# Kernel tuning notes

Hardware: AMD Instinct MI355X
Metric: run time of the kernel (lower is better)

Reference implementation:

```python
import jax, jax.numpy as jnp
import numpy as np
import math
from jax import lax

B, C, T = 32, 256, 1024
KS = 64          # key_size
KERN = 3         # conv kernel size
PAD = 2          # (KERN-1)*dilation, chomped -> causal left pad
SQRT_KS = math.sqrt(KS)


def setup_inputs() -> dict:
    key = jax.random.key(0)
    ks = jax.random.split(key, 14)
    s = 0.01
    return {
        "x":  jax.random.normal(ks[0], (B, C, T), jnp.float32),
        # attention linears (stored [in, out])
        "wq": jax.random.normal(ks[1], (C, KS), jnp.float32) * s,
        "bq": jnp.zeros((KS,), jnp.float32),
        "wk": jax.random.normal(ks[2], (C, KS), jnp.float32) * s,
        "bk": jnp.zeros((KS,), jnp.float32),
        "wv": jax.random.normal(ks[3], (C, C), jnp.float32) * s,
        "bv": jnp.zeros((C,), jnp.float32),
        # weight-normed conv 1: v [out,in,k], g [out], b [out]
        "v1": jax.random.normal(ks[4], (C, C, KERN), jnp.float32) * s,
        "g1": jnp.ones((C,), jnp.float32),
        "b1": jnp.zeros((C,), jnp.float32),
        # weight-normed conv 2
        "v2": jax.random.normal(ks[5], (C, C, KERN), jnp.float32) * s,
        "g2": jnp.ones((C,), jnp.float32),
        "b2": jnp.zeros((C,), jnp.float32),
    }


def _wn_conv_relu(h, v, g, b):
    # weight_norm (dim=0): W = g * v / ||v||, norm over (in, k) per out channel
    norm = jnp.sqrt(jnp.sum(v * v, axis=(1, 2), keepdims=True))
    W = (g[:, None, None] / norm) * v
    # left-pad PAD == Conv1d(padding=PAD) + Chomp1d(PAD)  (causal conv)
    y = lax.conv_general_dilated(h, W, window_strides=(1,), padding=[(PAD, 0)],
                                 dimension_numbers=("NCH", "OIH", "NCH"))
    return jax.nn.relu(y + b[None, :, None])


def reference(x, wq, bq, wk, bk, wv, bv, v1, g1, b1, v2, g2, b2):
    t = x.shape[2]
    xt = jnp.swapaxes(x, 1, 2)                      # [B, T, C]
    q = xt @ wq + bq                                # [B, T, KS]
    k = xt @ wk + bk                                # [B, T, KS]
    v = xt @ wv + bv                                # [B, T, C]
    scores = jnp.einsum("bqd,bkd->bqk", q, k)       # [B, Tq, Tk]
    # torch mask[j][i] = 1 if i > j -> masked where key index > query index
    idx = jnp.arange(t)
    mask = idx[None, :] > idx[:, None]              # [Tq, Tk]
    scores = jnp.where(mask[None], -jnp.inf, scores)
    # NOTE: source applies softmax over dim=1 (the QUERY axis) — faithful quirk
    attn = jax.nn.softmax(scores / SQRT_KS, axis=1)  # [B, Tq, Tk]
    out_attn = jnp.einsum("bqk,bkc->bqc", attn, v)  # [B, T, C]
    out_attn = jnp.swapaxes(out_attn, 1, 2)         # [B, C, T]
    # conv stack (dropout=0 / eval)
    out = _wn_conv_relu(out_attn, v1, g1, b1)
    out = _wn_conv_relu(out, v2, g2, b2)
    # en_res branch: per-timestep scaling of x by softmaxed attention mass
    weight_x = jax.nn.softmax(jnp.sum(attn, axis=2), axis=1)  # [B, T]
    en_res_x = weight_x[:, None, :] * x                       # [B, C, T]
    # downsample is None (n_inputs == n_outputs)
    return jax.nn.relu(out + x + en_res_x)
```

## Files before the change

kernel.cpp:

```cpp
#include <hip/hip_runtime.h>
#include <math.h>

#define BB 32
#define CC 256
#define TT 1024

typedef __attribute__((ext_vector_type(4))) float f4;
typedef __attribute__((ext_vector_type(4))) float f32x4;
typedef __attribute__((ext_vector_type(16))) float f32x16;
typedef __attribute__((ext_vector_type(8))) short s8;
typedef __attribute__((ext_vector_type(4))) short s4v;

__device__ inline short f2bf(float f) {
    unsigned u = __builtin_bit_cast(unsigned, f);
    u = (u + 0x7FFFu + ((u >> 16) & 1u)) >> 16;
    return (short)u;
}

static const size_t OFF_QBF  = 0;
static const size_t OFF_KBF  = 4194304;
static const size_t OFF_VT   = 8388608;
static const size_t OFF_OA   = 25165824;
static const size_t OFF_C1   = 58720256;
static const size_t OFF_CRZ  = 75497472;
static const size_t OFF_RS   = 75628544;
static const size_t OFF_WX   = 75759616;
static const size_t OFF_W1   = 75890688;
static const size_t OFF_W2   = 76283904;
static const size_t OFF_WQKV = 76677120;

__global__ __launch_bounds__(256)
void wn_kernel(const float* __restrict__ v1, const float* __restrict__ g1,
               const float* __restrict__ v2, const float* __restrict__ g2,
               short* __restrict__ w1bf, short* __restrict__ w2bf) {
    __shared__ float red[4];
    int which = blockIdx.x >> 8, o = blockIdx.x & 255;
    const float* v = which ? v2 : v1;
    const float* g = which ? g2 : g1;
    short* wt = which ? w2bf : w1bf;
    const float* row = v + (size_t)o * 768;
    int tid = threadIdx.x, lane = tid & 63, wv_ = tid >> 6;
    float r0 = row[tid], r1 = row[tid + 256], r2 = row[tid + 512];
    float s = r0 * r0 + r1 * r1 + r2 * r2;
    for (int d = 1; d < 64; d <<= 1) s += __shfl_xor(s, d, 64);
    if (lane == 0) red[wv_] = s;
    __syncthreads();
    float scale = g[o] * rsqrtf(red[0] + red[1] + red[2] + red[3]);
    for (int j = 0; j < 3; ++j)
        wt[((size_t)(j * 256 + o)) * 256 + tid] = f2bf(scale * row[tid * 3 + j]);
}

__global__ __launch_bounds__(256)
void pack_kernel(const float* __restrict__ wq, const float* __restrict__ wk,
                 const float* __restrict__ wv, short* __restrict__ wqkvbf) {
    int n = blockIdx.x * 4 + (threadIdx.x >> 6);
    int c0 = (threadIdx.x & 63) * 4;
    for (int p = 0; p < 4; ++p) {
        int c = c0 + p;
        float w;
        if (n < 64)       w = wq[c * 64 + n];
        else if (n < 128) w = wk[c * 64 + n - 64];
        else              w = wv[c * 256 + n - 128];
        wqkvbf[(size_t)n * 256 + c] = f2bf(w);
    }
}

__global__ void transpose_kernel(const float* __restrict__ x, short* __restrict__ xt) {
    __shared__ float Tt[64 * 68];
    int tid = threadIdx.x;
    int c0 = blockIdx.x * 64, t0 = blockIdx.y * 64, b = blockIdx.z;
    for (int it = 0; it < 4; ++it) {
        int idx = tid + 256 * it;
        int cr = idx >> 4, tc = idx & 15;
        f4 v = *reinterpret_cast<const f4*>(&x[((size_t)b * CC + c0 + cr) * TT + t0 + tc * 4]);
        *reinterpret_cast<f4*>(&Tt[cr * 68 + tc * 4]) = v;
    }
    __syncthreads();
    for (int it = 0; it < 2; ++it) {
        int idx = tid + 256 * it;
        int tl = idx >> 3, seg = idx & 7;
        s8 o;
        for (int p = 0; p < 8; ++p) o[p] = f2bf(Tt[(seg * 8 + p) * 68 + tl]);
        *reinterpret_cast<s8*>(&xt[((size_t)b * TT + t0 + tl) * CC + c0 + seg * 8]) = o;
    }
}

__global__ __launch_bounds__(256, 3)
void qkv_kernel(const short* __restrict__ xt, const short* __restrict__ wqkv,
                const float* __restrict__ bq, const float* __restrict__ bk,
                const float* __restrict__ bv,
                short* __restrict__ qbf, short* __restrict__ kbf, short* __restrict__ vt) {
    __shared__ short SL[128 * 72 + 64 * 72];
    short* Asm = SL;
    short* Bsm = SL + 128 * 72;
    int tid = threadIdx.x, wv_ = tid >> 6, lane = tid & 63;
    int n15 = lane & 15, quad = lane >> 4;
    int bid = blockIdx.x;
    int r = bid & 7, n = (bid >> 3) % 6, qd = bid / 48;
    int bt = qd * 8 + r;
    int b = bt >> 3, t0 = (bt & 7) * 128;
    int n0 = n * 64;

    f32x4 acc[2][4];
    for (int i = 0; i < 2; ++i) for (int j = 0; j < 4; ++j)
        for (int p = 0; p < 4; ++p) acc[i][j][p] = 0.f;

    for (int kc = 0; kc < 4; ++kc) {
        int c0 = kc * 64;
        __syncthreads();
        for (int it = 0; it < 4; ++it) {
            int idx = tid + 256 * it;
            int row = idx >> 3, seg = idx & 7;
            *reinterpret_cast<s8*>(&Asm[row * 72 + seg * 8]) =
                *reinterpret_cast<const s8*>(&xt[((size_t)b * TT + t0 + row) * CC + c0 + seg * 8]);
        }
        for (int it = 0; it < 2; ++it) {
            int idx = tid + 256 * it;
            int row = idx >> 3, seg = idx & 7;
            *reinterpret_cast<s8*>(&Bsm[row * 72 + seg * 8]) =
                *reinterpret_cast<const s8*>(&wqkv[(size_t)(n0 + row) * 256 + c0 + seg * 8]);
        }
        __syncthreads();
        for (int ks = 0; ks < 2; ++ks)
            for (int mt2 = 0; mt2 < 2; ++mt2) {
                s8 a = *reinterpret_cast<const s8*>(&Asm[(wv_ * 32 + mt2 * 16 + n15) * 72 + quad * 8 + ks * 32]);
                for (int nt = 0; nt < 4; ++nt) {
                    s8 bb = *reinterpret_cast<const s8*>(&Bsm[(nt * 16 + n15) * 72 + quad * 8 + ks * 32]);
                    acc[mt2][nt] = __builtin_amdgcn_mfma_f32_16x16x32_bf16(a, bb, acc[mt2][nt], 0, 0, 0);
                }
            }
    }
    if (n0 < 128) {
        short* outp = (n0 == 0) ? qbf : kbf;
        const float* bias = (n0 == 0) ? bq : bk;
        for (int mt2 = 0; mt2 < 2; ++mt2)
            for (int nt = 0; nt < 4; ++nt) {
                int n_ = nt * 16 + n15;
                float bvl = bias[n_];
                for (int reg = 0; reg < 4; ++reg) {
                    int t = t0 + wv_ * 32 + mt2 * 16 + quad * 4 + reg;
                    outp[((size_t)b * TT + t) * 64 + n_] = f2bf(acc[mt2][nt][reg] + bvl);
                }
            }
    } else {
        int cbase = n0 - 128;
        __syncthreads();
        short* Tw = SL + wv_ * 3072;
        for (int mt2 = 0; mt2 < 2; ++mt2)
            for (int nt = 0; nt < 4; ++nt) {
                int n_ = nt * 16 + n15;
                float bvl = bv[cbase + n_];
                for (int reg = 0; reg < 4; ++reg)
                    Tw[n_ * 48 + mt2 * 16 + quad * 4 + reg] = f2bf(acc[mt2][nt][reg] + bvl);
            }
        for (int p = 0; p < 4; ++p) {
            int n_ = (lane >> 2) + 16 * p;
            int seg = lane & 3;
            s8 vv = *reinterpret_cast<const s8*>(&Tw[n_ * 48 + seg * 8]);
            *reinterpret_cast<s8*>(&vt[((size_t)b * CC + cbase + n_) * TT + t0 + wv_ * 32 + seg * 8]) = vv;
        }
    }
}

__global__ __launch_bounds__(512, 2)
void colz_kernel(const short* __restrict__ qbf, const short* __restrict__ kbf,
                 float* __restrict__ colrz) {
    __shared__ short Qs[64 * 72], Ks[64 * 72];
    __shared__ float redz[8 * 32];
    int tid = threadIdx.x, wv_ = tid >> 6, lane = tid & 63;
    int l31 = lane & 31, lh = lane >> 5;
    int qhalf = wv_ & 1, khalf = (wv_ >> 1) & 1, w4 = wv_ >> 2;
    int bid = blockIdx.x;
    int half = bid >> 8;
    int idx = bid & 255;
    int b = idx >> 3, pr = idx & 7;
    int kt = half ? (15 - pr) : pr;
    int row = tid >> 3, sg = (tid & 7) * 8;

    s8 kr0 = *reinterpret_cast<const s8*>(&kbf[((size_t)b * TT + kt * 64 + row) * 64 + sg]);
    s8 qr0 = *reinterpret_cast<const s8*>(&qbf[((size_t)b * TT + kt * 64 + row) * 64 + sg]);
    float zloc = 0.f;
    for (int qt = kt; qt < 16; ++qt) {
        __syncthreads();
        if (qt == kt) *reinterpret_cast<s8*>(&Ks[row * 72 + sg]) = kr0;
        *reinterpret_cast<s8*>(&Qs[row * 72 + sg]) = qr0;
        __syncthreads();
        if (qt < 15)
            qr0 = *reinterpret_cast<const s8*>(&qbf[((size_t)b * TT + (qt + 1) * 64 + row) * 64 + sg]);
        f32x16 s;
        for (int p = 0; p < 16; ++p) s[p] = 0.f;
        for (int kc = 0; kc < 4; ++kc) {
            s8 a  = *reinterpret_cast<const s8*>(&Qs[(qhalf * 32 + l31) * 72 + kc * 16 + lh * 8]);
            s8 bb = *reinterpret_cast<const s8*>(&Ks[(khalf * 32 + l31) * 72 + kc * 16 + lh * 8]);
            s = __builtin_amdgcn_mfma_f32_32x32x16_bf16(a, bb, s, 0, 0, 0);
        }
        int kg = kt * 64 + khalf * 32 + l31;
        int qb0 = qt * 64 + qhalf * 32 + 4 * lh;
        if (qt > kt) {
            for (int r = 0; r < 8; ++r) {
                int reg = w4 * 8 + r;
                zloc += __expf(s[reg] * 0.125f);
            }
        } else {
            for (int r = 0; r < 8; ++r) {
                int reg = w4 * 8 + r;
                if (qb0 + (reg & 3) + 8 * (reg >> 2) >= kg) zloc += __expf(s[reg] * 0.125f);
            }
        }
    }
    float zc = zloc + __shfl_xor(zloc, 32, 64);
    if (lane < 32) redz[wv_ * 32 + lane] = zc;
    __syncthreads();
    if (tid < 64) {
        int kh = tid >> 5, kk = tid & 31;
        float Z;
        if (kh == 0) Z = redz[0 * 32 + kk] + redz[1 * 32 + kk] + redz[4 * 32 + kk] + redz[5 * 32 + kk];
        else         Z = redz[2 * 32 + kk] + redz[3 * 32 + kk] + redz[6 * 32 + kk] + redz[7 * 32 + kk];
        colrz[(size_t)b * TT + kt * 64 + tid] = 1.0f / Z;
    }
}

__global__ __launch_bounds__(512, 2)
void attn_kernel(const short* __restrict__ qbf, const short* __restrict__ kbf,
                 const short* __restrict__ vt, const float* __restrict__ colrz,
                 short* __restrict__ oab, float* __restrict__ rowsum) {
    __shared__ short Qs[64 * 72];
    __shared__ short Ks[64 * 72];
    __shared__ short Ps[64 * 72];
    __shared__ short Vs[256 * 72];
    __shared__ float redR[2][64];
    int tid = threadIdx.x, wv_ = tid >> 6, lane = tid & 63;
    int l31 = lane & 31, lh = lane >> 5;
    int wq2 = wv_ & 1, wk2 = (wv_ >> 1) & 1, w4 = wv_ >> 2, wcq = wv_ >> 1;
    int bid = blockIdx.x;
    int half = bid >> 8;
    int idx = bid & 255;
    int b = idx >> 3, pr = idx & 7;
    int qt = half ? pr : (15 - pr);
    int row = tid >> 3, sg = (tid & 7) * 8;

    s8 kreg, vreg[4];
    {
        kreg = *reinterpret_cast<const s8*>(&kbf[((size_t)b * TT + row) * 64 + sg]);
        for (int it = 0; it < 4; ++it) {
            int idx2 = tid + 512 * it;
            int vr = idx2 >> 3, seg = idx2 & 7;
            vreg[it] = *reinterpret_cast<const s8*>(&vt[((size_t)b * CC + vr) * TT + seg * 8]);
        }
    }

    s8 qr0 = *reinterpret_cast<const s8*>(&qbf[((size_t)b * TT + qt * 64 + row) * 64 + sg]);
    f32x16 acc[2];
    for (int i = 0; i < 2; ++i) for (int p = 0; p < 16; ++p) acc[i][p] = 0.f;
    float rsum[8];
    for (int i = 0; i < 8; ++i) rsum[i] = 0.f;

    for (int kt = 0; kt <= qt; ++kt) {
        __syncthreads();
        if (kt == 0) *reinterpret_cast<s8*>(&Qs[row * 72 + sg]) = qr0;
        *reinterpret_cast<s8*>(&Ks[row * 72 + sg]) = kreg;
        for (int it = 0; it < 4; ++it) {
            int idx2 = tid + 512 * it;
            int vr = idx2 >> 3, seg = idx2 & 7;
            *reinterpret_cast<s8*>(&Vs[vr * 72 + seg * 8]) = vreg[it];
        }
        __syncthreads();
        int nkt = (kt < qt) ? kt + 1 : -1;
        if (nkt >= 0) {
            kreg = *reinterpret_cast<const s8*>(&kbf[((size_t)b * TT + nkt * 64 + row) * 64 + sg]);
            for (int it = 0; it < 4; ++it) {
                int idx2 = tid + 512 * it;
                int vr = idx2 >> 3, seg = idx2 & 7;
                vreg[it] = *reinterpret_cast<const s8*>(&vt[((size_t)b * CC + vr) * TT + nkt * 64 + seg * 8]);
            }
        }
        f32x16 s;
        for (int p = 0; p < 16; ++p) s[p] = 0.f;
        for (int kc = 0; kc < 4; ++kc) {
            s8 a  = *reinterpret_cast<const s8*>(&Qs[(wq2 * 32 + l31) * 72 + kc * 16 + lh * 8]);
            s8 bb = *reinterpret_cast<const s8*>(&Ks[(wk2 * 32 + l31) * 72 + kc * 16 + lh * 8]);
            s = __builtin_amdgcn_mfma_f32_32x32x16_bf16(a, bb, s, 0, 0, 0);
        }
        int kg = kt * 64 + wk2 * 32 + l31;
        float rz = colrz[(size_t)b * TT + kg];
        bool full = (kt < qt);
        int qb0 = qt * 64 + wq2 * 32 + 4 * lh;
        for (int r = 0; r < 8; ++r) {
            int reg = w4 * 8 + r;
            int rr = (reg & 3) + 8 * (reg >> 2);
            float p = 0.f;
            if (full || qb0 + rr >= kg) p = __expf(s[reg] * 0.125f) * rz;
            rsum[r] += p;
            Ps[(wq2 * 32 + rr + 4 * lh) * 72 + wk2 * 32 + l31] = f2bf(p);
        }
        __syncthreads();
        for (int kc = 0; kc < 4; ++kc) {
            s8 a = *reinterpret_cast<const s8*>(&Ps[(wq2 * 32 + l31) * 72 + kc * 16 + lh * 8]);
            for (int nt = 0; nt < 2; ++nt) {
                s8 bb = *reinterpret_cast<const s8*>(&Vs[(wcq * 64 + nt * 32 + l31) * 72 + kc * 16 + lh * 8]);
                acc[nt] = __builtin_amdgcn_mfma_f32_32x32x16_bf16(a, bb, acc[nt], 0, 0, 0);
            }
        }
    }
    for (int r = 0; r < 8; ++r) {
        float v = rsum[r];
        v += __shfl_xor(v, 1, 64);
        v += __shfl_xor(v, 2, 64);
        v += __shfl_xor(v, 4, 64);
        v += __shfl_xor(v, 8, 64);
        v += __shfl_xor(v, 16, 64);
        int reg = w4 * 8 + r;
        int rr = (reg & 3) + 8 * (reg >> 2);
        if (l31 == 0) redR[wk2][wq2 * 32 + rr + 4 * lh] = v;
    }
    for (int nt = 0; nt < 2; ++nt) {
        int c = wcq * 64 + nt * 32 + l31;
        for (int reg = 0; reg < 16; ++reg) {
            int q = qt * 64 + wq2 * 32 + (reg & 3) + 8 * (reg >> 2) + 4 * lh;
            oab[((size_t)b * TT + q) * CC + c] = f2bf(acc[nt][reg]);
        }
    }
    __syncthreads();
    if (tid < 64) rowsum[(size_t)b * TT + qt * 64 + tid] = redR[0][tid] + redR[1][tid];
}

__global__ __launch_bounds__(256, 3)
void conv_kernel(const void* __restrict__ inp, int in_is_fp32,
                 const short* __restrict__ wbf, const float* __restrict__ bias,
                 void* __restrict__ outp, int out_is_bf16,
                 const float* __restrict__ xres, const float* __restrict__ wxv,
                 int fuse_final) {
    __shared__ short SL[130 * 72 + 3 * 64 * 72];
    short* As = SL;
    short* Bs = SL + 130 * 72;
    int tid = threadIdx.x, wv_ = tid >> 6, lane = tid & 63;
    int n15 = lane & 15, quad = lane >> 4;
    int bid = blockIdx.x;
    int r = bid & 7;
    int n0 = ((bid >> 3) & 3) << 6;
    int bm = (bid >> 5) * 8 + r;
    int b = bm >> 3, mt = bm & 7;
    int t0 = mt * 128;
    f32x4 acc[2][4];
    for (int i = 0; i < 2; ++i) for (int j = 0; j < 4; ++j)
        for (int p = 0; p < 4; ++p) acc[i][j][p] = 0.f;

    for (int kc = 0; kc < 4; ++kc) {
        int c0 = kc * 64;
        __syncthreads();
        if (in_is_fp32) {
            const float* in = (const float*)inp;
            for (int it = 0; it < 9; ++it) {
                int idx = tid + 256 * it;
                int row = idx >> 4, fc = idx & 15;
                if (row < 130) {
                    int t = t0 + row - 2;
                    s4v st;
                    if (t >= 0) {
                        f4 v = *reinterpret_cast<const f4*>(&in[((size_t)b * TT + t) * CC + c0 + fc * 4]);
                        for (int p = 0; p < 4; ++p) st[p] = f2bf(v[p]);
                    } else { for (int p = 0; p < 4; ++p) st[p] = 0; }
                    *reinterpret_cast<s4v*>(&As[row * 72 + fc * 4]) = st;
                }
            }
        } else {
            const short* in = (const short*)inp;
            for (int it = 0; it < 5; ++it) {
                int idx = tid + 256 * it;
                int row = idx >> 3, seg = idx & 7;
                if (row < 130) {
                    int t = t0 + row - 2;
                    s8 st;
                    if (t >= 0) st = *reinterpret_cast<const s8*>(&in[((size_t)b * TT + t) * CC + c0 + seg * 8]);
                    else for (int p = 0; p < 8; ++p) st[p] = 0;
                    *reinterpret_cast<s8*>(&As[row * 72 + seg * 8]) = st;
                }
            }
        }
        for (int it = 0; it < 6; ++it) {
            int idx = tid + 256 * it;
            int row = idx >> 3, seg = idx & 7;
            int j = row >> 6, o = row & 63;
            *reinterpret_cast<s8*>(&Bs[row * 72 + seg * 8]) =
                *reinterpret_cast<const s8*>(&wbf[((size_t)(j * 256 + n0 + o)) * 256 + c0 + seg * 8]);
        }
        __syncthreads();
        for (int j = 0; j < 3; ++j)
            for (int ks = 0; ks < 2; ++ks)
                for (int mt2 = 0; mt2 < 2; ++mt2) {
                    s8 a = *reinterpret_cast<const s8*>(&As[(wv_ * 32 + mt2 * 16 + n15 + j) * 72 + quad * 8 + ks * 32]);
                    for (int nt = 0; nt < 4; ++nt) {
                        s8 bb = *reinterpret_cast<const s8*>(&Bs[(j * 64 + nt * 16 + n15) * 72 + quad * 8 + ks * 32]);
                        acc[mt2][nt] = __builtin_amdgcn_mfma_f32_16x16x32_bf16(a, bb, acc[mt2][nt], 0, 0, 0);
                    }
                }
    }
    if (!fuse_final) {
        for (int mt2 = 0; mt2 < 2; ++mt2)
            for (int nt = 0; nt < 4; ++nt) {
                int o = n0 + nt * 16 + n15;
                float bvl = bias[o];
                for (int reg = 0; reg < 4; ++reg) {
                    int t = t0 + wv_ * 32 + mt2 * 16 + quad * 4 + reg;
                    float v = fmaxf(acc[mt2][nt][reg] + bvl, 0.f);
                    if (out_is_bf16) ((short*)outp)[((size_t)b * TT + t) * CC + o] = f2bf(v);
                    else             ((float*)outp)[((size_t)b * TT + t) * CC + o] = v;
                }
            }
    } else {
        float* Ft = (float*)SL;
        __syncthreads();
        for (int mt2 = 0; mt2 < 2; ++mt2)
            for (int nt = 0; nt < 4; ++nt) {
                int ol = nt * 16 + n15;
                float bvl = bias[n0 + ol];
                for (int reg = 0; reg < 4; ++reg) {
                    int tl = wv_ * 32 + mt2 * 16 + quad * 4 + reg;
                    Ft[tl * 67 + ol] = fmaxf(acc[mt2][nt][reg] + bvl, 0.f);
                }
            }
        __syncthreads();
        int c_l = tid >> 5;
        int t_l = (tid & 31) * 4;
        f4 wv4 = *reinterpret_cast<const f4*>(&wxv[(size_t)b * TT + t0 + t_l]);
        for (int pass = 0; pass < 8; ++pass) {
            int c = n0 + pass * 8 + c_l;
            f4 xv = *reinterpret_cast<const f4*>(&xres[((size_t)b * CC + c) * TT + t0 + t_l]);
            f4 rr;
            for (int p = 0; p < 4; ++p)
                rr[p] = fmaxf(Ft[(t_l + p) * 67 + pass * 8 + c_l] + xv[p] * (1.f + wv4[p]), 0.f);
            *reinterpret_cast<f4*>(&((float*)outp)[((size_t)b * CC + c) * TT + t0 + t_l]) = rr;
        }
    }
}

__global__ void rowsm_kernel(const float* __restrict__ rowsum, float* __restrict__ wx) {
    __shared__ float red[256];
    int b = blockIdx.x, tid = threadIdx.x;
    float v[4];
    float m = -1e30f;
    for (int r = 0; r < 4; ++r) { v[r] = rowsum[(size_t)b * TT + tid + 256 * r]; m = fmaxf(m, v[r]); }
    red[tid] = m; __syncthreads();
    for (int s = 128; s > 0; s >>= 1) { if (tid < s) red[tid] = fmaxf(red[tid], red[tid + s]); __syncthreads(); }
    m = red[0]; __syncthreads();
    float e[4], zs = 0.f;
    for (int r = 0; r < 4; ++r) { e[r] = __expf(v[r] - m); zs += e[r]; }
    red[tid] = zs; __syncthreads();
    for (int s = 128; s > 0; s >>= 1) { if (tid < s) red[tid] += red[tid + s]; __syncthreads(); }
    float rz = 1.0f / red[0];
    for (int r = 0; r < 4; ++r) wx[(size_t)b * TT + tid + 256 * r] = e[r] * rz;
}

extern "C" void kernel_launch(void* const* d_in, const int* in_sizes, int n_in,
                              void* d_out, int out_size, void* d_ws, size_t ws_size,
                              hipStream_t stream) {
    (void)in_sizes; (void)n_in; (void)out_size; (void)ws_size;
    const float* x  = (const float*)d_in[0];
    const float* wq = (const float*)d_in[1];
    const float* bq = (const float*)d_in[2];
    const float* wk = (const float*)d_in[3];
    const float* bk = (const float*)d_in[4];
    const float* wv = (const float*)d_in[5];
    const float* bv = (const float*)d_in[6];
    const float* v1 = (const float*)d_in[7];
    const float* g1 = (const float*)d_in[8];
    const float* b1 = (const float*)d_in[9];
    const float* v2 = (const float*)d_in[10];
    const float* g2 = (const float*)d_in[11];
    const float* b2 = (const float*)d_in[12];
    char* ws = (char*)d_ws;
    float* out = (float*)d_out;

    short* qbf  = (short*)(ws + OFF_QBF);
    short* kbf  = (short*)(ws + OFF_KBF);
    short* vt   = (short*)(ws + OFF_VT);
    short* xt   = (short*)(ws + OFF_OA);
    short* oab  = (short*)(ws + OFF_OA);
    short* c1   = (short*)(ws + OFF_C1);
    float* crz  = (float*)(ws + OFF_CRZ);
    float* rs   = (float*)(ws + OFF_RS);
    float* wxb  = (float*)(ws + OFF_WX);
    short* w1bf = (short*)(ws + OFF_W1);
    short* w2bf = (short*)(ws + OFF_W2);
    short* wqkv = (short*)(ws + OFF_WQKV);

    wn_kernel<<<dim3(512), dim3(256), 0, stream>>>(v1, g1, v2, g2, w1bf, w2bf);
    pack_kernel<<<dim3(96), dim3(256), 0, stream>>>(wq, wk, wv, wqkv);
    transpose_kernel<<<dim3(4, 16, 32), dim3(256), 0, stream>>>(x, xt);
    qkv_kernel<<<dim3(1536), dim3(256), 0, stream>>>(xt, wqkv, bq, bk, bv, qbf, kbf, vt);
    colz_kernel<<<dim3(512), dim3(512), 0, stream>>>(qbf, kbf, crz);
    attn_kernel<<<dim3(512), dim3(512), 0, stream>>>(qbf, kbf, vt, crz, oab, rs);
    rowsm_kernel<<<dim3(32), dim3(256), 0, stream>>>(rs, wxb);
    conv_kernel<<<dim3(1024), dim3(256), 0, stream>>>(oab, 0, w1bf, b1, c1, 1,
                                                      nullptr, nullptr, 0);
    conv_kernel<<<dim3(1024), dim3(256), 0, stream>>>(c1, 0, w2bf, b2, out, 0,
                                                      x, wxb, 1);
}
```

Measured before the change: 251.8 us.

## Restructure attention and column-normalizer kernels to load MFMA fragments from global directly

Both colz and attn kernels now read Q/K/V MFMA operand fragments straight from global memory into registers, dropping the shared-memory staging of Q, K and V. Each block now handles two paired tiles (pr and 15-pr) for causal load balance, and the query tile is split into 32-row halves across blocks. attn uses a double-buffered P tile with one barrier per iteration, and launch bounds go up to four blocks per SM for occupancy. In exchange, K and V fragments are re-read from global/L2 by more blocks and waves, and the exp work is spread across duplicate waves.

```diff
diff --git a/kernel.cpp b/kernel.cpp
--- a/kernel.cpp
+++ b/kernel.cpp
@@ -162,166 +162,151 @@
     }
 }
 
-__global__ __launch_bounds__(512, 2)
+__global__ __launch_bounds__(512, 4)
 void colz_kernel(const short* __restrict__ qbf, const short* __restrict__ kbf,
                  float* __restrict__ colrz) {
-    __shared__ short Qs[64 * 72], Ks[64 * 72];
     __shared__ float redz[8 * 32];
     int tid = threadIdx.x, wv_ = tid >> 6, lane = tid & 63;
     int l31 = lane & 31, lh = lane >> 5;
-    int qhalf = wv_ & 1, khalf = (wv_ >> 1) & 1, w4 = wv_ >> 2;
+    int qhf = wv_ & 1, wdup = wv_ >> 1;
     int bid = blockIdx.x;
-    int half = bid >> 8;
+    int kh = bid >> 8;
     int idx = bid & 255;
     int b = idx >> 3, pr = idx & 7;
-    int kt = half ? (15 - pr) : pr;
-    int row = tid >> 3, sg = (tid & 7) * 8;
-
-    s8 kr0 = *reinterpret_cast<const s8*>(&kbf[((size_t)b * TT + kt * 64 + row) * 64 + sg]);
-    s8 qr0 = *reinterpret_cast<const s8*>(&qbf[((size_t)b * TT + kt * 64 + row) * 64 + sg]);
-    float zloc = 0.f;
-    for (int qt = kt; qt < 16; ++qt) {
-        __syncthreads();
-        if (qt == kt) *reinterpret_cast<s8*>(&Ks[row * 72 + sg]) = kr0;
-        *reinterpret_cast<s8*>(&Qs[row * 72 + sg]) = qr0;
-        __syncthreads();
-        if (qt < 15)
-            qr0 = *reinterpret_cast<const s8*>(&qbf[((size_t)b * TT + (qt + 1) * 64 + row) * 64 + sg]);
-        f32x16 s;
-        for (int p = 0; p < 16; ++p) s[p] = 0.f;
-        for (int kc = 0; kc < 4; ++kc) {
-            s8 a  = *reinterpret_cast<const s8*>(&Qs[(qhalf * 32 + l31) * 72 + kc * 16 + lh * 8]);
-            s8 bb = *reinterpret_cast<const s8*>(&Ks[(khalf * 32 + l31) * 72 + kc * 16 + lh * 8]);
-            s = __builtin_amdgcn_mfma_f32_32x32x16_bf16(a, bb, s, 0, 0, 0);
-        }
-        int kg = kt * 64 + khalf * 32 + l31;
-        int qb0 = qt * 64 + qhalf * 32 + 4 * lh;
-        if (qt > kt) {
-            for (int r = 0; r < 8; ++r) {
-                int reg = w4 * 8 + r;
-                zloc += __expf(s[reg] * 0.125f);
-            }
-        } else {
-            for (int r = 0; r < 8; ++r) {
-                int reg = w4 * 8 + r;
-                if (qb0 + (reg & 3) + 8 * (reg >> 2) >= kg) zloc += __expf(s[reg] * 0.125f);
-            }
-        }
-    }
-    float zc = zloc + __shfl_xor(zloc, 32, 64);
-    if (lane < 32) redz[wv_ * 32 + lane] = zc;
-    __syncthreads();
-    if (tid < 64) {
-        int kh = tid >> 5, kk = tid & 31;
-        float Z;
-        if (kh == 0) Z = redz[0 * 32 + kk] + redz[1 * 32 + kk] + redz[4 * 32 + kk] + redz[5 * 32 + kk];
-        else         Z = redz[2 * 32 + kk] + redz[3 * 32 + kk] + redz[6 * 32 + kk] + redz[7 * 32 + kk];
-        colrz[(size_t)b * TT + kt * 64 + tid] = 1.0f / Z;
-    }
-}
-
-__global__ __launch_bounds__(512, 2)
+    int kts[2] = {pr, 15 - pr};
+    const short* qb = qbf + (size_t)b * TT * 64;
+    const short* kb = kbf + (size_t)b * TT * 64;
+
+    for (int ph = 0; ph < 2; ++ph) {
+        int kt = kts[ph];
+        s8 kf[4], qf[4];
+        for (int kc = 0; kc < 4; ++kc)
+            kf[kc] = *reinterpret_cast<const s8*>(
+                &kb[(size_t)(kt * 64 + kh * 32 + l31) * 64 + kc * 16 + lh * 8]);
+        for (int kc = 0; kc < 4; ++kc)
+            qf[kc] = *reinterpret_cast<const s8*>(
+                &qb[(size_t)(kt * 64 + qhf * 32 + l31) * 64 + kc * 16 + lh * 8]);
+        float zloc = 0.f;
+        int kg = kt * 64 + kh * 32 + l31;
+        for (int qt = kt; qt < 16; ++qt) {
+            f32x16 s;
+            for (int p = 0; p < 16; ++p) s[p] = 0.f;
+            for (int kc = 0; kc < 4; ++kc)
+                s = __builtin_amdgcn_mfma_f32_32x32x16_bf16(qf[kc], kf[kc], s, 0, 0, 0);
+            if (qt < 15)
+                for (int kc = 0; kc < 4; ++kc)
+                    qf[kc] = *reinterpret_cast<const s8*>(
+                        &qb[(size_t)((qt + 1) * 64 + qhf * 32 + l31) * 64 + kc * 16 + lh * 8]);
+            int qg0 = qt * 64 + qhf * 32 + 4 * lh + 8 * wdup;
+            if (qt > kt) {
+                for (int r = 0; r < 4; ++r)
+                    zloc += __expf(s[wdup * 4 + r] * 0.125f);
+            } else {
+                for (int r = 0; r < 4; ++r)
+                    if (qg0 + r >= kg) zloc += __expf(s[wdup * 4 + r] * 0.125f);
+            }
+        }
+        float zc = zloc + __shfl_xor(zloc, 32, 64);
+        if (lane < 32) redz[wv_ * 32 + lane] = zc;
+        __syncthreads();
+        if (tid < 32) {
+            float Z = 0.f;
+            for (int w = 0; w < 8; ++w) Z += redz[w * 32 + tid];
+            colrz[(size_t)b * TT + kt * 64 + kh * 32 + tid] = 1.0f / Z;
+        }
+        __syncthreads();
+    }
+}
+
+__global__ __launch_bounds__(512, 4)
 void attn_kernel(const short* __restrict__ qbf, const short* __restrict__ kbf,
                  const short* __restrict__ vt, const float* __restrict__ colrz,
                  short* __restrict__ oab, float* __restrict__ rowsum) {
-    __shared__ short Qs[64 * 72];
-    __shared__ short Ks[64 * 72];
-    __shared__ short Ps[64 * 72];
-    __shared__ short Vs[256 * 72];
-    __shared__ float redR[2][64];
+    __shared__ short Ps[2][32 * 72];
+    __shared__ float redR[2][32];
     int tid = threadIdx.x, wv_ = tid >> 6, lane = tid & 63;
     int l31 = lane & 31, lh = lane >> 5;
-    int wq2 = wv_ & 1, wk2 = (wv_ >> 1) & 1, w4 = wv_ >> 2, wcq = wv_ >> 1;
+    int wk2 = wv_ & 1, wdup = wv_ >> 1;
     int bid = blockIdx.x;
-    int half = bid >> 8;
+    int qh = bid >> 8;
     int idx = bid & 255;
     int b = idx >> 3, pr = idx & 7;
-    int qt = half ? pr : (15 - pr);
-    int row = tid >> 3, sg = (tid & 7) * 8;
-
-    s8 kreg, vreg[4];
-    {
-        kreg = *reinterpret_cast<const s8*>(&kbf[((size_t)b * TT + row) * 64 + sg]);
-        for (int it = 0; it < 4; ++it) {
-            int idx2 = tid + 512 * it;
-            int vr = idx2 >> 3, seg = idx2 & 7;
-            vreg[it] = *reinterpret_cast<const s8*>(&vt[((size_t)b * CC + vr) * TT + seg * 8]);
-        }
-    }
-
-    s8 qr0 = *reinterpret_cast<const s8*>(&qbf[((size_t)b * TT + qt * 64 + row) * 64 + sg]);
-    f32x16 acc[2];
-    for (int i = 0; i < 2; ++i) for (int p = 0; p < 16; ++p) acc[i][p] = 0.f;
-    float rsum[8];
-    for (int i = 0; i < 8; ++i) rsum[i] = 0.f;
-
-    for (int kt = 0; kt <= qt; ++kt) {
-        __syncthreads();
-        if (kt == 0) *reinterpret_cast<s8*>(&Qs[row * 72 + sg]) = qr0;
-        *reinterpret_cast<s8*>(&Ks[row * 72 + sg]) = kreg;
-        for (int it = 0; it < 4; ++it) {
-            int idx2 = tid + 512 * it;
-            int vr = idx2 >> 3, seg = idx2 & 7;
-            *reinterpret_cast<s8*>(&Vs[vr * 72 + seg * 8]) = vreg[it];
-        }
-        __syncthreads();
-        int nkt = (kt < qt) ? kt + 1 : -1;
-        if (nkt >= 0) {
-            kreg = *reinterpret_cast<const s8*>(&kbf[((size_t)b * TT + nkt * 64 + row) * 64 + sg]);
-            for (int it = 0; it < 4; ++it) {
-                int idx2 = tid + 512 * it;
-                int vr = idx2 >> 3, seg = idx2 & 7;
-                vreg[it] = *reinterpret_cast<const s8*>(&vt[((size_t)b * CC + vr) * TT + nkt * 64 + seg * 8]);
-            }
-        }
-        f32x16 s;
-        for (int p = 0; p < 16; ++p) s[p] = 0.f;
-        for (int kc = 0; kc < 4; ++kc) {
-            s8 a  = *reinterpret_cast<const s8*>(&Qs[(wq2 * 32 + l31) * 72 + kc * 16 + lh * 8]);
-            s8 bb = *reinterpret_cast<const s8*>(&Ks[(wk2 * 32 + l31) * 72 + kc * 16 + lh * 8]);
-            s = __builtin_amdgcn_mfma_f32_32x32x16_bf16(a, bb, s, 0, 0, 0);
-        }
-        int kg = kt * 64 + wk2 * 32 + l31;
-        float rz = colrz[(size_t)b * TT + kg];
-        bool full = (kt < qt);
-        int qb0 = qt * 64 + wq2 * 32 + 4 * lh;
-        for (int r = 0; r < 8; ++r) {
-            int reg = w4 * 8 + r;
-            int rr = (reg & 3) + 8 * (reg >> 2);
-            float p = 0.f;
-            if (full || qb0 + rr >= kg) p = __expf(s[reg] * 0.125f) * rz;
-            rsum[r] += p;
-            Ps[(wq2 * 32 + rr + 4 * lh) * 72 + wk2 * 32 + l31] = f2bf(p);
-        }
-        __syncthreads();
-        for (int kc = 0; kc < 4; ++kc) {
-            s8 a = *reinterpret_cast<const s8*>(&Ps[(wq2 * 32 + l31) * 72 + kc * 16 + lh * 8]);
-            for (int nt = 0; nt < 2; ++nt) {
-                s8 bb = *reinterpret_cast<const s8*>(&Vs[(wcq * 64 + nt * 32 + l31) * 72 + kc * 16 + lh * 8]);
-                acc[nt] = __builtin_amdgcn_mfma_f32_32x32x16_bf16(a, bb, acc[nt], 0, 0, 0);
-            }
-        }
-    }
-    for (int r = 0; r < 8; ++r) {
-        float v = rsum[r];
-        v += __shfl_xor(v, 1, 64);
-        v += __shfl_xor(v, 2, 64);
-        v += __shfl_xor(v, 4, 64);
-        v += __shfl_xor(v, 8, 64);
-        v += __shfl_xor(v, 16, 64);
-        int reg = w4 * 8 + r;
-        int rr = (reg & 3) + 8 * (reg >> 2);
-        if (l31 == 0) redR[wk2][wq2 * 32 + rr + 4 * lh] = v;
-    }
-    for (int nt = 0; nt < 2; ++nt) {
-        int c = wcq * 64 + nt * 32 + l31;
+    int qts[2] = {15 - pr, pr};
+
+    const short* qb = qbf + (size_t)b * TT * 64;
+    const short* kb = kbf + (size_t)b * TT * 64;
+    const short* vb = vt + (size_t)b * CC * TT;
+
+    s8 kf[4], vf[4];
+    for (int kc = 0; kc < 4; ++kc) {
+        kf[kc] = *reinterpret_cast<const s8*>(
+            &kb[(size_t)(wk2 * 32 + l31) * 64 + kc * 16 + lh * 8]);
+        vf[kc] = *reinterpret_cast<const s8*>(
+            &vb[(size_t)(wv_ * 32 + l31) * TT + kc * 16 + lh * 8]);
+    }
+    int pp = 0;
+    for (int ph = 0; ph < 2; ++ph) {
+        int qt = qts[ph];
+        s8 qf[4];
+        for (int kc = 0; kc < 4; ++kc)
+            qf[kc] = *reinterpret_cast<const s8*>(
+                &qb[(size_t)(qt * 64 + qh * 32 + l31) * 64 + kc * 16 + lh * 8]);
+        f32x16 acc;
+        for (int p = 0; p < 16; ++p) acc[p] = 0.f;
+        float rsum[4] = {0.f, 0.f, 0.f, 0.f};
+
+        for (int kt = 0; kt <= qt; ++kt) {
+            f32x16 s;
+            for (int p = 0; p < 16; ++p) s[p] = 0.f;
+            for (int kc = 0; kc < 4; ++kc)
+                s = __builtin_amdgcn_mfma_f32_32x32x16_bf16(qf[kc], kf[kc], s, 0, 0, 0);
+            int nkt = (kt < qt) ? kt + 1 : ((ph == 0) ? 0 : -1);
+            if (nkt >= 0)
+                for (int kc = 0; kc < 4; ++kc)
+                    kf[kc] = *reinterpret_cast<const s8*>(
+                        &kb[(size_t)(nkt * 64 + wk2 * 32 + l31) * 64 + kc * 16 + lh * 8]);
+            int kg = kt * 64 + wk2 * 32 + l31;
+            float rz = colrz[(size_t)b * TT + kg];
+            bool full = (kt < qt);
+            int qg0 = qt * 64 + qh * 32 + 4 * lh + 8 * wdup;
+            short* Pw = Ps[pp];
+            for (int r = 0; r < 4; ++r) {
+                int reg = wdup * 4 + r;
+                float p = 0.f;
+                if (full || qg0 + r >= kg) p = __expf(s[reg] * 0.125f) * rz;
+                rsum[r] += p;
+                Pw[(8 * wdup + r + 4 * lh) * 72 + wk2 * 32 + l31] = f2bf(p);
+            }
+            __syncthreads();
+            const short* Pr = Ps[pp];
+            for (int kc = 0; kc < 4; ++kc) {
+                s8 a = *reinterpret_cast<const s8*>(&Pr[l31 * 72 + kc * 16 + lh * 8]);
+                acc = __builtin_amdgcn_mfma_f32_32x32x16_bf16(a, vf[kc], acc, 0, 0, 0);
+            }
+            if (nkt >= 0)
+                for (int kc = 0; kc < 4; ++kc)
+                    vf[kc] = *reinterpret_cast<const s8*>(
+                        &vb[(size_t)(wv_ * 32 + l31) * TT + nkt * 64 + kc * 16 + lh * 8]);
+            pp ^= 1;
+        }
+        int c = wv_ * 32 + l31;
         for (int reg = 0; reg < 16; ++reg) {
-            int q = qt * 64 + wq2 * 32 + (reg & 3) + 8 * (reg >> 2) + 4 * lh;
-            oab[((size_t)b * TT + q) * CC + c] = f2bf(acc[nt][reg]);
-        }
-    }
-    __syncthreads();
-    if (tid < 64) rowsum[(size_t)b * TT + qt * 64 + tid] = redR[0][tid] + redR[1][tid];
+            int q = qt * 64 + qh * 32 + (reg & 3) + 8 * (reg >> 2) + 4 * lh;
+            oab[((size_t)b * TT + q) * CC + c] = f2bf(acc[reg]);
+        }
+        for (int r = 0; r < 4; ++r) {
+            float v = rsum[r];
+            v += __shfl_xor(v, 1, 64);
+            v += __shfl_xor(v, 2, 64);
+            v += __shfl_xor(v, 4, 64);
+            v += __shfl_xor(v, 8, 64);
+            v += __shfl_xor(v, 16, 64);
+            if (l31 == 0) redR[wk2][8 * wdup + r + 4 * lh] = v;
+        }
+        __syncthreads();
+        if (tid < 32)
+            rowsum[(size_t)b * TT + qt * 64 + qh * 32 + tid] = redR[0][tid] + redR[1][tid];
+    }
 }
 
 __global__ __launch_bounds__(256, 3)
```

After: 297.3 us. 18.0% more time.
